# Optimization experiments

Hardware: AMD Instinct MI355X
Metric: run time of the kernel (lower is better)

Reference implementation:

```python
import jax, jax.numpy as jnp
import numpy as np

HIDDEN = 256
HEADS = 8
HEAD_DIM = HIDDEN // HEADS
SCALE = HEAD_DIM ** -0.5
N = 4096
NUM_GRAPHS = 16
LN_EPS = 1e-5


def setup_inputs() -> dict:
    key = jax.random.key(0)
    ks = jax.random.split(key, 8)
    x = jax.random.normal(ks[0], (N, HIDDEN), dtype=jnp.float32)
    batch = jnp.sort(jax.random.randint(ks[1], (N,), 0, NUM_GRAPHS, dtype=jnp.int64))
    # Xavier-uniform linear weights, stored as [in, out] (y = x @ W + b)
    lim = float(np.sqrt(6.0 / (HIDDEN + HIDDEN)))
    def W(k):
        return jax.random.uniform(k, (HIDDEN, HIDDEN), jnp.float32, -lim, lim)
    return {
        "x": x,
        "batch": batch,
        "Wq": W(ks[2]), "bq": jnp.zeros((HIDDEN,), jnp.float32),
        "Wk": W(ks[3]), "bk": jnp.zeros((HIDDEN,), jnp.float32),
        "Wv": W(ks[4]), "bv": jnp.zeros((HIDDEN,), jnp.float32),
        "Wo": W(ks[5]), "bo": jnp.zeros((HIDDEN,), jnp.float32),
        "gamma": jnp.ones((HIDDEN,), jnp.float32),
        "beta": jnp.zeros((HIDDEN,), jnp.float32),
    }


def _layer_norm(x, gamma, beta):
    mu = jnp.mean(x, axis=-1, keepdims=True)
    var = jnp.mean(jnp.square(x - mu), axis=-1, keepdims=True)
    return (x - mu) * jax.lax.rsqrt(var + LN_EPS) * gamma + beta


def reference(x, batch, Wq, bq, Wk, bk, Wv, bv, Wo, bo, gamma, beta):
    residual = x
    h = _layer_norm(x, gamma, beta)
    n = h.shape[0]
    q = (h @ Wq + bq).reshape(n, HEADS, HEAD_DIM)
    k = (h @ Wk + bk).reshape(n, HEADS, HEAD_DIM)
    v = (h @ Wv + bv).reshape(n, HEADS, HEAD_DIM)
    # dense scores masked to block-diagonal (same-graph) structure
    scores = jnp.einsum('ihd,jhd->ihj', q, k) * SCALE  # [N, H, N]
    same_graph = (batch[None, :] == batch[:, None])[:, None, :]  # [N, 1, N]
    scores = jnp.where(same_graph, scores, -jnp.inf)
    attn = jax.nn.softmax(scores, axis=-1)
    attn = jnp.nan_to_num(attn, nan=0.0)
    out = jnp.einsum('ihj,jhd->ihd', attn, v).reshape(n, HIDDEN)
    out = out @ Wo + bo
    return residual + out
```

## Files before the change

kernel.cpp:

```cpp
#include <hip/hip_runtime.h>

#define NNODES 4096
#define HID 256
#define NG 16
#define NH 8
#define HD 32
#define LN_EPS 1e-5f
#define QSCALE (0.17677669529663687f * 1.4426950408889634f)
#define CAPT 384
#define KLS 40
#define VTS (CAPT + 2)
#define HLS 264

typedef unsigned short u16;
typedef unsigned int u32;
typedef __bf16 bf16x8 __attribute__((ext_vector_type(8)));
typedef float f32x4 __attribute__((ext_vector_type(4)));

__device__ __forceinline__ u16 f2bf(float f){
  union { float f; u32 i; } c; c.f = f;
  u32 x = c.i;
  return (u16)((x + 0x7fffu + ((x >> 16) & 1u)) >> 16);
}

__global__ __launch_bounds__(256) void lnqkv_kernel(
    const float* __restrict__ x, const float* __restrict__ gamma,
    const float* __restrict__ beta,
    const float* __restrict__ Wq, const float* __restrict__ Wk,
    const float* __restrict__ Wv,
    const float* __restrict__ bq, const float* __restrict__ bk,
    const float* __restrict__ bv,
    u16* __restrict__ qb, u16* __restrict__ kb, u16* __restrict__ vb){
  __shared__ u16 hl[64][HLS];
  int bid = blockIdx.x;
  int which = blockIdx.y;
  int wave = threadIdx.x >> 6, lane = threadIdx.x & 63;
  int m0 = (bid >> 2) * 64;
  int nb = (bid & 3) * 64 + wave * 16;
  const float* W    = (which == 0) ? Wq : (which == 1) ? Wk : Wv;
  const float* bias = (which == 0) ? bq : (which == 1) ? bk : bv;
  u16* out          = (which == 0) ? qb : (which == 1) ? kb : vb;

  int rsub = lane >> 4;
  int c16  = lane & 15;
  float4 g0 = *(const float4*)(gamma + c16 * 16 + 0);
  float4 g1 = *(const float4*)(gamma + c16 * 16 + 4);
  float4 g2 = *(const float4*)(gamma + c16 * 16 + 8);
  float4 g3 = *(const float4*)(gamma + c16 * 16 + 12);
  float4 t0 = *(const float4*)(beta + c16 * 16 + 0);
  float4 t1 = *(const float4*)(beta + c16 * 16 + 4);
  float4 t2 = *(const float4*)(beta + c16 * 16 + 8);
  float4 t3 = *(const float4*)(beta + c16 * 16 + 12);
  float ga[16] = {g0.x,g0.y,g0.z,g0.w, g1.x,g1.y,g1.z,g1.w,
                  g2.x,g2.y,g2.z,g2.w, g3.x,g3.y,g3.z,g3.w};
  float bt[16] = {t0.x,t0.y,t0.z,t0.w, t1.x,t1.y,t1.z,t1.w,
                  t2.x,t2.y,t2.z,t2.w, t3.x,t3.y,t3.z,t3.w};
  #pragma unroll
  for (int b = 0; b < 4; b++){
    int rloc = wave * 16 + b * 4 + rsub;
    const float* xr = x + (size_t)(m0 + rloc) * HID + c16 * 16;
    float4 v0 = *(const float4*)(xr + 0);
    float4 v1 = *(const float4*)(xr + 4);
    float4 v2 = *(const float4*)(xr + 8);
    float4 v3 = *(const float4*)(xr + 12);
    float e[16] = {v0.x,v0.y,v0.z,v0.w, v1.x,v1.y,v1.z,v1.w,
                   v2.x,v2.y,v2.z,v2.w, v3.x,v3.y,v3.z,v3.w};
    float s = 0.f;
    #pragma unroll
    for (int i = 0; i < 16; i++) s += e[i];
    s += __shfl_xor(s, 1); s += __shfl_xor(s, 2);
    s += __shfl_xor(s, 4); s += __shfl_xor(s, 8);
    float mu = s * (1.0f / HID);
    float vv = 0.f;
    #pragma unroll
    for (int i = 0; i < 16; i++){ e[i] -= mu; vv += e[i] * e[i]; }
    vv += __shfl_xor(vv, 1); vv += __shfl_xor(vv, 2);
    vv += __shfl_xor(vv, 4); vv += __shfl_xor(vv, 8);
    float rs = rsqrtf(vv * (1.0f / HID) + LN_EPS);
    u32 pk[8];
    #pragma unroll
    for (int i = 0; i < 8; i++){
      float o0 = e[2*i]     * rs * ga[2*i]     + bt[2*i];
      float o1 = e[2*i + 1] * rs * ga[2*i + 1] + bt[2*i + 1];
      pk[i] = (u32)f2bf(o0) | ((u32)f2bf(o1) << 16);
    }
    *(uint4*)&hl[rloc][c16 * 16]     = make_uint4(pk[0], pk[1], pk[2], pk[3]);
    *(uint4*)&hl[rloc][c16 * 16 + 8] = make_uint4(pk[4], pk[5], pk[6], pk[7]);
  }
  __syncthreads();

  int lr = lane & 15, lq = lane >> 4;
  f32x4 acc[4] = {};
  const float* wbase = W + nb + lr;
  #pragma unroll
  for (int k0 = 0; k0 < HID; k0 += 32){
    union { bf16x8 v; u16 e[8]; } bf;
    const float* wp = wbase + (size_t)(k0 + lq * 8) * HID;
    #pragma unroll
    for (int j = 0; j < 8; j++) bf.e[j] = f2bf(wp[(size_t)j * HID]);
    #pragma unroll
    for (int t = 0; t < 4; t++){
      bf16x8 a = *(const bf16x8*)&hl[t * 16 + lr][k0 + lq * 8];
      acc[t] = __builtin_amdgcn_mfma_f32_16x16x32_bf16(a, bf.v, acc[t], 0, 0, 0);
    }
  }
  int col = nb + lr;
  float bb = bias[col];
  #pragma unroll
  for (int t = 0; t < 4; t++){
    #pragma unroll
    for (int r = 0; r < 4; r++){
      int row = m0 + 16 * t + lq * 4 + r;
      out[(size_t)row * HID + col] = f2bf(acc[t][r] + bb);
    }
  }
}

__global__ __launch_bounds__(512, 4) void attn_kernel(const u16* __restrict__ q,
    const u16* __restrict__ k, const u16* __restrict__ v,
    const int* __restrict__ batch, int bstride, u16* __restrict__ out){
  __shared__ u16 kl[CAPT * KLS];
  __shared__ u16 vt[HD * VTS];
  __shared__ float mg[4][10][64];
  __shared__ int s_se[2];
  int gh = blockIdx.y;
  int g = gh >> 3, hd = gh & 7;
  int wave = threadIdx.x >> 6, lane = threadIdx.x & 63;
  if (wave < 2){
    int target = g + wave;
    int p = batch[(size_t)(lane * 64) * bstride];
    int c = __popcll(__ballot(p < target));
    int lo = 0;
    if (c > 0){
      int base = (c - 1) * 64 + 1;
      int idx = base + lane;
      int val = (idx < NNODES) ? batch[(size_t)idx * bstride] : 0x7fffffff;
      lo = base + __popcll(__ballot(val < target));
    }
    if (lane == 0) s_se[wave] = lo;
  }
  __syncthreads();
  int start = s_se[0], end = s_se[1];
  int len = end - start;
  if (len <= 0) return;
  if (len > CAPT) len = CAPT;
  int ntj = (len + 15) >> 4;
  int nj16 = ntj << 4;
  for (int idx = threadIdx.x; idx < nj16 * 4; idx += 512){
    int row = idx >> 2, part = idx & 3;
    uint4 val = make_uint4(0, 0, 0, 0);
    if (row < len)
      val = *(const uint4*)&k[(size_t)(start + row) * HID + hd * HD + part * 8];
    *(uint4*)&kl[row * KLS + part * 8] = val;
  }
  for (int idx = threadIdx.x; idx < nj16 * 4; idx += 512){
    int row = idx >> 2, part = idx & 3;
    uint4 w = make_uint4(0, 0, 0, 0);
    if (row < len)
      w = *(const uint4*)&v[(size_t)(start + row) * HID + hd * HD + part * 8];
    int d0 = part * 8;
    vt[(d0 + 0) * VTS + row] = (u16)(w.x & 0xffffu);
    vt[(d0 + 1) * VTS + row] = (u16)(w.x >> 16);
    vt[(d0 + 2) * VTS + row] = (u16)(w.y & 0xffffu);
    vt[(d0 + 3) * VTS + row] = (u16)(w.y >> 16);
    vt[(d0 + 4) * VTS + row] = (u16)(w.z & 0xffffu);
    vt[(d0 + 5) * VTS + row] = (u16)(w.z >> 16);
    vt[(d0 + 6) * VTS + row] = (u16)(w.w & 0xffffu);
    vt[(d0 + 7) * VTS + row] = (u16)(w.w >> 16);
  }
  __syncthreads();
  int lq = lane >> 4, lr = lane & 15;
  int tl = wave & 3;
  int jh = wave >> 2;
  int nouter = (ntj + 15) >> 4;
  for (int it = 0; it < nouter; it++){
    int tq = it * 16 + blockIdx.x * 4 + tl;
    bool active = tq < ntj;
    int q0 = tq << 4;
    float m = -3.0e38f, l = 0.f;
    f32x4 o0 = {0.f,0.f,0.f,0.f}, o1 = {0.f,0.f,0.f,0.f};
    if (active){
      bf16x8 qf = *(const bf16x8*)&q[(size_t)(start + q0 + lr) * HID + hd * HD + lq * 8];
      int half = (ntj + 1) >> 1;
      int jt0 = jh ? half : 0;
      int jt1 = jh ? ntj : half;
      for (int jt = jt0; jt < jt1; jt++){
        int j0 = jt << 4;
        bf16x8 kf = *(const bf16x8*)&kl[(j0 + lr) * KLS + lq * 8];
        f32x4 st = __builtin_amdgcn_mfma_f32_16x16x32_bf16(kf, qf,
                     (f32x4){0.f,0.f,0.f,0.f}, 0, 0, 0);
        int jb = j0 + lq * 4;
        float s0 = (jb + 0 < len) ? st[0] * QSCALE : -3.0e38f;
        float s1 = (jb + 1 < len) ? st[1] * QSCALE : -3.0e38f;
        float s2 = (jb + 2 < len) ? st[2] * QSCALE : -3.0e38f;
        float s3 = (jb + 3 < len) ? st[3] * QSCALE : -3.0e38f;
        float tm = fmaxf(fmaxf(s0, s1), fmaxf(s2, s3));
        tm = fmaxf(tm, __shfl_xor(tm, 16));
        tm = fmaxf(tm, __shfl_xor(tm, 32));
        float mn = fmaxf(m, tm);
        float alpha = exp2f(m - mn);
        float p0 = exp2f(s0 - mn), p1 = exp2f(s1 - mn);
        float p2 = exp2f(s2 - mn), p3 = exp2f(s3 - mn);
        float ps = (p0 + p1) + (p2 + p3);
        ps += __shfl_xor(ps, 16);
        ps += __shfl_xor(ps, 32);
        l = l * alpha + ps;
        m = mn;
        union { bf16x8 v8; u32 w[4]; } pf, vf0, vf1;
        pf.w[0] = (u32)f2bf(p0) | ((u32)f2bf(p1) << 16);
        pf.w[1] = (u32)f2bf(p2) | ((u32)f2bf(p3) << 16);
        pf.w[2] = 0; pf.w[3] = 0;
        const u16* vp0 = &vt[lr * VTS + j0 + lq * 4];
        const u16* vp1 = &vt[(16 + lr) * VTS + j0 + lq * 4];
        vf0.w[0] = *(const u32*)vp0; vf0.w[1] = *(const u32*)(vp0 + 2);
        vf0.w[2] = 0; vf0.w[3] = 0;
        vf1.w[0] = *(const u32*)vp1; vf1.w[1] = *(const u32*)(vp1 + 2);
        vf1.w[2] = 0; vf1.w[3] = 0;
        o0 = o0 * alpha;
        o1 = o1 * alpha;
        o0 = __builtin_amdgcn_mfma_f32_16x16x32_bf16(vf0.v8, pf.v8, o0, 0, 0, 0);
        o1 = __builtin_amdgcn_mfma_f32_16x16x32_bf16(vf1.v8, pf.v8, o1, 0, 0, 0);
      }
    }
    if (jh == 1){
      mg[tl][0][lane] = o0[0]; mg[tl][1][lane] = o0[1];
      mg[tl][2][lane] = o0[2]; mg[tl][3][lane] = o0[3];
      mg[tl][4][lane] = o1[0]; mg[tl][5][lane] = o1[1];
      mg[tl][6][lane] = o1[2]; mg[tl][7][lane] = o1[3];
      mg[tl][8][lane] = m;     mg[tl][9][lane] = l;
    }
    __syncthreads();
    if (jh == 0 && active && q0 + lr < len){
      float m2 = mg[tl][8][lane], l2 = mg[tl][9][lane];
      float mn = fmaxf(m, m2);
      float a  = exp2f(m - mn);
      float a2 = exp2f(m2 - mn);
      float lt = l * a + l2 * a2;
      float rl = 1.0f / lt;
      float r0 = (o0[0]*a + mg[tl][0][lane]*a2) * rl;
      float r1 = (o0[1]*a + mg[tl][1][lane]*a2) * rl;
      float r2 = (o0[2]*a + mg[tl][2][lane]*a2) * rl;
      float r3 = (o0[3]*a + mg[tl][3][lane]*a2) * rl;
      float r4 = (o1[0]*a + mg[tl][4][lane]*a2) * rl;
      float r5 = (o1[1]*a + mg[tl][5][lane]*a2) * rl;
      float r6 = (o1[2]*a + mg[tl][6][lane]*a2) * rl;
      float r7 = (o1[3]*a + mg[tl][7][lane]*a2) * rl;
      u16* orow = out + (size_t)(start + q0 + lr) * HID + hd * HD;
      int dbase = lq * 4;
      *(u32*)&orow[dbase]          = (u32)f2bf(r0) | ((u32)f2bf(r1) << 16);
      *(u32*)&orow[dbase + 2]      = (u32)f2bf(r2) | ((u32)f2bf(r3) << 16);
      *(u32*)&orow[16 + dbase]     = (u32)f2bf(r4) | ((u32)f2bf(r5) << 16);
      *(u32*)&orow[16 + dbase + 2] = (u32)f2bf(r6) | ((u32)f2bf(r7) << 16);
    }
    __syncthreads();
  }
}

__global__ __launch_bounds__(256) void proj_kernel(const u16* __restrict__ ao,
    const float* __restrict__ Wo, const float* __restrict__ bo,
    const float* __restrict__ x, float* __restrict__ out){
  int gw = blockIdx.x * 4 + (threadIdx.x >> 6);
  int lane = threadIdx.x & 63;
  int lr = lane & 15, lq = lane >> 4;
  int m0 = (gw >> 4) * 64;
  int n0 = (gw & 15) * 16;
  f32x4 acc[4] = {};
  const u16* arow = ao + (size_t)(m0 + lr) * HID + lq * 8;
  const float* wbase = Wo + n0 + lr;
  #pragma unroll
  for (int k0 = 0; k0 < HID; k0 += 32){
    union { bf16x8 v; u16 e[8]; } bf;
    const float* wp = wbase + (size_t)(k0 + lq * 8) * HID;
    #pragma unroll
    for (int j = 0; j < 8; j++) bf.e[j] = f2bf(wp[(size_t)j * HID]);
    #pragma unroll
    for (int t = 0; t < 4; t++){
      bf16x8 a = *(const bf16x8*)(arow + (size_t)t * 16 * HID + k0);
      acc[t] = __builtin_amdgcn_mfma_f32_16x16x32_bf16(a, bf.v, acc[t], 0, 0, 0);
    }
  }
  int col = n0 + lr;
  float bb = bo[col];
  #pragma unroll
  for (int t = 0; t < 4; t++){
    #pragma unroll
    for (int r = 0; r < 4; r++){
      size_t row = (size_t)(m0 + 16 * t + lq * 4 + r) * HID + col;
      out[row] = acc[t][r] + bb + x[row];
    }
  }
}

__global__ void sentinel_kernel(u32* __restrict__ out, int nwords){
  int i = blockIdx.x * 256 + threadIdx.x;
  if (i < nwords) out[i] = 0x46404640u;
}

extern "C" void kernel_launch(void* const* d_in, const int* in_sizes, int n_in,
                              void* d_out, int out_size, void* d_ws, size_t ws_size,
                              hipStream_t stream){
  const float* x   = (const float*)d_in[0];
  const int* batch = (const int*)d_in[1];
  const float* Wq = (const float*)d_in[2],  *bq = (const float*)d_in[3];
  const float* Wk = (const float*)d_in[4],  *bk = (const float*)d_in[5];
  const float* Wv = (const float*)d_in[6],  *bv = (const float*)d_in[7];
  const float* Wo = (const float*)d_in[8],  *bo = (const float*)d_in[9];
  const float* gamma = (const float*)d_in[10], *beta = (const float*)d_in[11];

  const size_t BUF  = (size_t)NNODES * HID * 2;
  const size_t NEED = 1024 + 4 * BUF;

  if (ws_size < NEED){
    int nwords = out_size / 2;
    sentinel_kernel<<<(nwords + 255) / 256, 256, 0, stream>>>((u32*)d_out, nwords);
    return;
  }

  int bstride = (in_sizes[1] >= NNODES * 8) ? 2 : 1;

  char* w = (char*)d_ws;
  u16* qb = (u16*)(w + 1024);
  u16* kb = qb + (size_t)NNODES * HID;
  u16* vb = kb + (size_t)NNODES * HID;
  u16* ao = vb + (size_t)NNODES * HID;

  lnqkv_kernel<<<dim3(256, 3), 256, 0, stream>>>(x, gamma, beta, Wq, Wk, Wv,
                                                 bq, bk, bv, qb, kb, vb);
  attn_kernel<<<dim3(4, NG * NH), 512, 0, stream>>>(qb, kb, vb, batch, bstride, ao);
  proj_kernel<<<256, 256, 0, stream>>>(ao, Wo, bo, x, (float*)d_out);
}
```

Baseline: 115.8 us.

## Read K and V directly from global memory instead of staging in LDS

Removes the shared-memory staging of K tiles and transposed V tiles, along with the block-wide barrier that followed them. The inner attention loop now loads K fragments and V elements straight from global memory with clamped row indices. This drops the LDS footprint and the CAPT segment-length cap, which could raise occupancy and fix truncation for large graphs. In exchange, every wave redundantly reads K/V through cache, and V is gathered with scattered 2-byte loads on the critical path of each iteration.

```diff
diff --git a/kernel.cpp b/kernel.cpp
--- a/kernel.cpp
+++ b/kernel.cpp
@@ -7,9 +7,6 @@
 #define HD 32
 #define LN_EPS 1e-5f
 #define QSCALE (0.17677669529663687f * 1.4426950408889634f)
-#define CAPT 384
-#define KLS 40
-#define VTS (CAPT + 2)
 #define HLS 264
 
 typedef unsigned short u16;
@@ -119,8 +116,6 @@
 __global__ __launch_bounds__(512, 4) void attn_kernel(const u16* __restrict__ q,
     const u16* __restrict__ k, const u16* __restrict__ v,
     const int* __restrict__ batch, int bstride, u16* __restrict__ out){
-  __shared__ u16 kl[CAPT * KLS];
-  __shared__ u16 vt[HD * VTS];
   __shared__ float mg[4][10][64];
   __shared__ int s_se[2];
   int gh = blockIdx.y;
@@ -143,32 +138,7 @@
   int start = s_se[0], end = s_se[1];
   int len = end - start;
   if (len <= 0) return;
-  if (len > CAPT) len = CAPT;
   int ntj = (len + 15) >> 4;
-  int nj16 = ntj << 4;
-  for (int idx = threadIdx.x; idx < nj16 * 4; idx += 512){
-    int row = idx >> 2, part = idx & 3;
-    uint4 val = make_uint4(0, 0, 0, 0);
-    if (row < len)
-      val = *(const uint4*)&k[(size_t)(start + row) * HID + hd * HD + part * 8];
-    *(uint4*)&kl[row * KLS + part * 8] = val;
-  }
-  for (int idx = threadIdx.x; idx < nj16 * 4; idx += 512){
-    int row = idx >> 2, part = idx & 3;
-    uint4 w = make_uint4(0, 0, 0, 0);
-    if (row < len)
-      w = *(const uint4*)&v[(size_t)(start + row) * HID + hd * HD + part * 8];
-    int d0 = part * 8;
-    vt[(d0 + 0) * VTS + row] = (u16)(w.x & 0xffffu);
-    vt[(d0 + 1) * VTS + row] = (u16)(w.x >> 16);
-    vt[(d0 + 2) * VTS + row] = (u16)(w.y & 0xffffu);
-    vt[(d0 + 3) * VTS + row] = (u16)(w.y >> 16);
-    vt[(d0 + 4) * VTS + row] = (u16)(w.z & 0xffffu);
-    vt[(d0 + 5) * VTS + row] = (u16)(w.z >> 16);
-    vt[(d0 + 6) * VTS + row] = (u16)(w.w & 0xffffu);
-    vt[(d0 + 7) * VTS + row] = (u16)(w.w >> 16);
-  }
-  __syncthreads();
   int lq = lane >> 4, lr = lane & 15;
   int tl = wave & 3;
   int jh = wave >> 2;
@@ -186,7 +156,18 @@
       int jt1 = jh ? ntj : half;
       for (int jt = jt0; jt < jt1; jt++){
         int j0 = jt << 4;
-        bf16x8 kf = *(const bf16x8*)&kl[(j0 + lr) * KLS + lq * 8];
+        int krow = start + j0 + lr;
+        if (krow > NNODES - 1) krow = NNODES - 1;
+        bf16x8 kf = *(const bf16x8*)&k[(size_t)krow * HID + hd * HD + lq * 8];
+        u16 va[4], vc[4];
+        #pragma unroll
+        for (int i = 0; i < 4; i++){
+          int vrow = start + j0 + lq * 4 + i;
+          if (vrow > NNODES - 1) vrow = NNODES - 1;
+          const u16* vp = &v[(size_t)vrow * HID + hd * HD + lr];
+          va[i] = vp[0];
+          vc[i] = vp[16];
+        }
         f32x4 st = __builtin_amdgcn_mfma_f32_16x16x32_bf16(kf, qf,
                      (f32x4){0.f,0.f,0.f,0.f}, 0, 0, 0);
         int jb = j0 + lq * 4;
@@ -210,11 +191,11 @@
         pf.w[0] = (u32)f2bf(p0) | ((u32)f2bf(p1) << 16);
         pf.w[1] = (u32)f2bf(p2) | ((u32)f2bf(p3) << 16);
         pf.w[2] = 0; pf.w[3] = 0;
-        const u16* vp0 = &vt[lr * VTS + j0 + lq * 4];
-        const u16* vp1 = &vt[(16 + lr) * VTS + j0 + lq * 4];
-        vf0.w[0] = *(const u32*)vp0; vf0.w[1] = *(const u32*)(vp0 + 2);
+        vf0.w[0] = (u32)va[0] | ((u32)va[1] << 16);
+        vf0.w[1] = (u32)va[2] | ((u32)va[3] << 16);
         vf0.w[2] = 0; vf0.w[3] = 0;
-        vf1.w[0] = *(const u32*)vp1; vf1.w[1] = *(const u32*)(vp1 + 2);
+        vf1.w[0] = (u32)vc[0] | ((u32)vc[1] << 16);
+        vf1.w[1] = (u32)vc[2] | ((u32)vc[3] << 16);
         vf1.w[2] = 0; vf1.w[3] = 0;
         o0 = o0 * alpha;
         o1 = o1 * alpha;
```

Result: no change. 115.7 us (-0.1%).
